# Performance work log

Hardware: AMD Instinct MI355X
Metric: run time of the kernel (lower is better)

## Reference

```python
import jax, jax.numpy as jnp
import numpy as np

# ---- p4m group tables (g = 4*m + r, m in {0,1} mirror, r in {0..3} rot90) ----
def _p4m_tables():
    R = np.array([[0, -1], [1, 0]])
    F = np.array([[-1, 0], [0, 1]])
    I = np.eye(2, dtype=int)
    mats = []
    for m in (0, 1):
        for r in range(4):
            mats.append(np.linalg.matrix_power(R, r) @ (F if m else I))
    def idx(M):
        for i, A in enumerate(mats):
            if np.array_equal(A, M):
                return i
        raise ValueError('not in group')
    comp = np.array([[idx(mats[a] @ mats[b]) for b in range(8)] for a in range(8)])
    inv = np.array([idx(mats[a].T) for a in range(8)])  # orthogonal -> inv = transpose
    return comp, inv

COMP, INV = _p4m_tables()

def _transform_kernel(g, W):
    # L_g applied to filter spatial axes: mirror (last axis) then rotate r times
    m, r = g // 4, g % 4
    if m:
        W = jnp.flip(W, axis=-1)
    return jnp.rot90(W, k=r, axes=(-2, -1))

STRIDE, PADDING, DILATION = 1, 1, 1

def setup_inputs() -> dict:
    key = jax.random.key(0)
    k1, k2 = jax.random.split(key)
    B, Cin, Cout, H, W, kH, kW = 16, 64, 64, 64, 64, 3, 3
    x = jax.random.normal(k1, (B, Cin, 8, H, W), dtype=jnp.float32)
    scale = 1.0 / np.sqrt(Cin * kH * kW)
    weight_rel = jax.random.normal(k2, (Cout, Cin, 8, kH, kW), dtype=jnp.float32) * scale
    bias = jnp.zeros((Cout,), dtype=jnp.float32)
    return {'x': x, 'weight_rel': weight_rel, 'bias': bias}

def _gconv(x, weight_rel, bias):
    B, Cin, N, H, Wd = x.shape  # N == 8
    Cout, _, _, kH, kW = weight_rel.shape
    # Build the full group-equivariant filter bank once (fused form of the
    # original 64 small conv2d calls): bank[g*Cout+co, c*8+h] = L_g psi(g^{-1} h)
    banks = []
    for g in range(8):
        u = COMP[INV[g]]                # [8] relative element u = g^{-1} h, for h=0..7
        Wg = weight_rel[:, :, u]        # [Cout, Cin, 8, kH, kW]
        banks.append(_transform_kernel(g, Wg))
    bank = jnp.stack(banks, 0)          # [8, Cout, Cin, 8, kH, kW]
    bank = bank.reshape(8 * Cout, Cin * 8, kH, kW)
    x2 = x.reshape(B, Cin * 8, H, Wd)   # in-channel index = c*8 + h, matches bank
    y = jax.lax.conv_general_dilated(
        x2, bank,
        window_strides=(STRIDE, STRIDE),
        padding=[(PADDING, PADDING), (PADDING, PADDING)],
        rhs_dilation=(DILATION, DILATION),
        dimension_numbers=('NCHW', 'OIHW', 'NCHW'))
    Ho, Wo = y.shape[-2], y.shape[-1]
    y = y.reshape(B, 8, Cout, Ho, Wo).transpose(0, 2, 1, 3, 4)  # [B, Cout, 8, Ho, Wo]
    return y + bias[None, :, None, None, None]

def reference(x, weight_rel, bias):
    return _gconv(x, weight_rel, bias)
```

## Files before the change

### kernel.cpp

```cpp
#include <hip/hip_runtime.h>
#include <stdint.h>

typedef short  bf16x8 __attribute__((ext_vector_type(8)));
typedef float  f32x4  __attribute__((ext_vector_type(4)));


__device__ __forceinline__ short f2bf(float f) {
    uint32_t u = __builtin_bit_cast(uint32_t, f);
    u += 0x7FFFu + ((u >> 16) & 1u);
    return (short)(u >> 16);
}

__device__ __forceinline__ int u_index(int g, int s) {
    int r  = g & 3, m  = g >> 2;
    int r2 = s & 3, ms = s >> 2;
    if (!m) { int rr = (r2 - r) & 3; return ms ? (4 + rr) : rr; }
    else    { int rr = (r - r2) & 3; return ms ? rr : (4 + rr); }
}

__device__ __forceinline__ void gload_lds16(const void* g, void* l) {
    __builtin_amdgcn_global_load_lds(
        (const __attribute__((address_space(1))) uint32_t*)g,
        (__attribute__((address_space(3))) uint32_t*)l, 16, 0, 0);
}

#define XB_BYTES  (16LL * 66 * 66 * 512 * 2)
#define BK_BYTES  (16LL * 9 * 4 * 512 * 8 * 2)
#define WS_NEEDED (XB_BYTES + BK_BYTES)


__global__ __launch_bounds__(256) void prep_x2(const float* __restrict__ x,
                                               short* __restrict__ xb) {
    __shared__ float t[64][65];
    const int h = blockIdx.x, kc8 = blockIdx.y, b = blockIdx.z;
    const int k0 = kc8 * 64;
    const int tid = threadIdx.x;
    const int w  = tid & 63, kq = tid >> 6;
    const float* xp = x + ((size_t)(b * 512 + k0 + kq) * 4096) + h * 64 + w;
    #pragma unroll
    for (int i = 0; i < 16; ++i)
        t[kq + 4 * i][w] = xp[(size_t)(4 * i) * 4096];
    __syncthreads();
    const int w2 = tid >> 3, kk = tid & 7;
    #pragma unroll
    for (int half = 0; half < 2; ++half) {
        const int ww = w2 + 32 * half;
        bf16x8 v;
        #pragma unroll
        for (int j = 0; j < 8; ++j) v[j] = f2bf(t[kk * 8 + j][ww]);
        size_t o = (((size_t)b * 66 + h + 1) * 66 + (ww + 1)) * 512 + k0 + kk * 8;
        *reinterpret_cast<bf16x8*>(&xb[o]) = v;
    }
}

__global__ __launch_bounds__(256) void zero_border(short* __restrict__ xb) {
    int idx = blockIdx.x * 256 + threadIdx.x;
    if (idx >= 16 * 260 * 64) return;
    int kg = idx & 63;
    int rest = idx >> 6;
    int b  = rest / 260;
    int pe = rest - b * 260;
    int hh, ww;
    if      (pe < 66)  { hh = 0;            ww = pe; }
    else if (pe < 132) { hh = 65;           ww = pe - 66; }
    else if (pe < 196) { hh = pe - 132 + 1; ww = 0; }
    else               { hh = pe - 196 + 1; ww = 65; }
    size_t o = (((size_t)b * 66 + hh) * 66 + ww) * 512 + kg * 8;
    bf16x8 z = {0,0,0,0,0,0,0,0};
    *reinterpret_cast<bf16x8*>(&xb[o]) = z;
}

__global__ __launch_bounds__(256) void prep_w(const float* __restrict__ wrel,
                                              short* __restrict__ bank) {
    int tg = blockIdx.x * 256 + threadIdx.x;
    int oc = tg & 511;
    int kg = (tg >> 9) & 3;
    int kc = (tg >> 11) & 15;
    int t  = tg >> 15;
    int ki = t / 3, kj = t - ki * 3;
    int g = oc & 7, co = oc >> 3;
    int r = g & 3, m = g >> 2;
    int a0, b0;
    switch (r) {
        case 0:  a0 = ki;     b0 = kj;     break;
        case 1:  a0 = kj;     b0 = 2 - ki; break;
        case 2:  a0 = 2 - ki; b0 = 2 - kj; break;
        default: a0 = 2 - kj; b0 = ki;     break;
    }
    if (m) b0 = 2 - b0;
    int ci = kc * 4 + kg;
    const float* wp = wrel + (size_t)(co * 64 + ci) * 72 + a0 * 3 + b0;
    bf16x8 v;
    #pragma unroll
    for (int j = 0; j < 8; ++j) v[j] = f2bf(wp[u_index(g, j) * 9]);
    size_t o = (((((size_t)kc * 3 + kj) * 3 + ki) * 4 + kg) * 512 + oc) * 8;
    *reinterpret_cast<bf16x8*>(&bank[o]) = v;
}

#define XS_SH (1344 * 8)
#define WB_SH (768 * 8)

#define STAGE_X(XS, kc)                                                    \
    {                                                                      \
        _Pragma("unroll")                                                  \
        for (int q = 0; q < 6; ++q) {                                      \
            int it = wid + 4 * q;                                          \
            if (it < 21)                                                   \
                gload_lds16(xb + (size_t)xoff[q] + (kc) * 32,              \
                            &XS[it * 512]);                                \
        }                                                                  \
    }

#define STAGE_W(WB, kc, kj)                                                \
    {                                                                      \
        _Pragma("unroll")                                                  \
        for (int q = 0; q < 3; ++q) {                                      \
            int it = wid + 4 * q;                                          \
            gload_lds16(bank + (size_t)((kc) * 3 + (kj)) * 49152           \
                             + woff[q],                                    \
                        &WB[it * 512]);                                    \
        }                                                                  \
    }

#define COMPUTE_KJ(XS, WB, kj)                                             \
    {                                                                      \
        bf16x8 bfr[6];                                                     \
        _Pragma("unroll")                                                  \
        for (int rr = 0; rr < 6; ++rr)                                     \
            bfr[rr] = *reinterpret_cast<const bf16x8*>(                    \
                &XS[(lkg * 336 + (wid * 4 + rr) * 18 + l15 + (kj)) * 8]);  \
        _Pragma("unroll")                                                  \
        for (int ki = 0; ki < 3; ++ki) {                                   \
            bf16x8 a[4];                                                   \
            _Pragma("unroll")                                              \
            for (int mi = 0; mi < 4; ++mi)                                 \
                a[mi] = *reinterpret_cast<const bf16x8*>(                  \
                    &WB[((ki * 4 + lkg) * 64 + mi * 16 + l15) * 8]);       \
            _Pragma("unroll")                                              \
            for (int nj = 0; nj < 4; ++nj) {                               \
                bf16x8 bv = bfr[nj + ki];                                  \
                _Pragma("unroll")                                          \
                for (int mi = 0; mi < 4; ++mi)                             \
                    acc[mi][nj] = __builtin_amdgcn_mfma_f32_16x16x32_bf16( \
                        a[mi], bv, acc[mi][nj], 0, 0, 0);                  \
            }                                                              \
        }                                                                  \
    }

#define CHUNK(kc, XC, XN, W0, W1)                                          \
    {                                                                      \
        STAGE_W(W1, kc, 1);                                                \
        COMPUTE_KJ(XC, W0, 0);                                             \
        __syncthreads();                                                   \
        STAGE_W(W0, kc, 2);                                                \
        if ((kc) < 15) STAGE_X(XN, (kc) + 1);                              \
        COMPUTE_KJ(XC, W1, 1);                                             \
        __syncthreads();                                                   \
        if ((kc) < 15) STAGE_W(W1, (kc) + 1, 0);                           \
        COMPUTE_KJ(XC, W0, 2);                                             \
        __syncthreads();                                                   \
    }

__global__ __launch_bounds__(256, 2) void gconv_mfma(
    const short* __restrict__ xb, const short* __restrict__ bank,
    const float* __restrict__ bias, float* __restrict__ out)
{
    __shared__ __attribute__((aligned(16))) short xsA[XS_SH], xsB[XS_SH];
    __shared__ __attribute__((aligned(16))) short wbA[WB_SH], wbB[WB_SH];

    const int st  = blockIdx.x;
    const int ot  = blockIdx.y;
    const int b   = blockIdx.z;
    const int h0  = (st >> 2) * 16;
    const int w0  = (st & 3) * 16;
    const int oc0 = ot * 64;

    const int tid  = threadIdx.x;
    const int lane = tid & 63;
    const int wid  = tid >> 6;
    const int l15  = lane & 15;
    const int lkg  = lane >> 4;

    f32x4 acc[4][4];
    #pragma unroll
    for (int i = 0; i < 4; ++i)
        #pragma unroll
        for (int j = 0; j < 4; ++j)
            #pragma unroll
            for (int e = 0; e < 4; ++e) acc[i][j][e] = 0.f;

    const int xrow_base = (b * 66 + h0) * 66 + w0;

    int xoff[6];
    #pragma unroll
    for (int q = 0; q < 6; ++q) {
        int it = wid + 4 * q;
        if (it > 20) it = 20;
        int slot = it * 64 + lane;
        int kg = slot / 336;
        int px = slot - kg * 336;
        px = px < 324 ? px : 323;
        int r = px / 18;
        int c = px - r * 18;
        xoff[q] = (xrow_base + r * 66 + c) * 512 + kg * 8;
    }
    int woff[3];
    #pragma unroll
    for (int q = 0; q < 3; ++q) {
        int it = wid + 4 * q;
        woff[q] = (it * 512 + oc0 + lane) * 8;
    }

    STAGE_X(xsA, 0);
    STAGE_W(wbA, 0, 0);
    __syncthreads();
    for (int kc2 = 0; kc2 < 8; ++kc2) {
        CHUNK(2 * kc2,     xsA, xsB, wbA, wbB);
        CHUNK(2 * kc2 + 1, xsB, xsA, wbB, wbA);
    }

    #pragma unroll
    for (int mi = 0; mi < 4; ++mi) {
        #pragma unroll
        for (int j = 0; j < 4; ++j) {
            const int oc_g = oc0 + mi * 16 + lkg * 4 + j;
            const float bv = bias[oc_g >> 3];
            float* op = out + ((size_t)b * 512 + oc_g) * 4096;
            #pragma unroll
            for (int nj = 0; nj < 4; ++nj) {
                const int hh = h0 + wid * 4 + nj;
                op[hh * 64 + w0 + l15] = acc[mi][nj][j] + bv;
            }
        }
    }
}

__global__ __launch_bounds__(256) void gconv_direct(
    const float* __restrict__ x, const float* __restrict__ wrel,
    const float* __restrict__ bias, float* __restrict__ out)
{
    __shared__ float xsf[18][20];
    __shared__ float wsf[16][9];
    const int st = blockIdx.x, ct = blockIdx.y, b = blockIdx.z;
    const int h0 = (st >> 2) * 16, w0 = (st & 3) * 16, oc0 = ct * 16;
    const int tid = threadIdx.x;
    const int ch = tid & 15, blk = tid >> 4;
    const int by = (blk >> 2) * 4, bx = (blk & 3) * 4;
    const int oc = oc0 + ch, g = oc & 7, co = oc >> 3;
    const int wl_c = tid / 9, wl_k = tid - wl_c * 9;
    const int wl_i = wl_k / 3, wl_j = wl_k - wl_i * 3;
    const int wl_oc = oc0 + wl_c, wl_g = wl_oc & 7, wl_co = wl_oc >> 3;
    int a0, b0;
    { const int r = wl_g & 3, m = wl_g >> 2;
      switch (r) { case 0: a0=wl_i; b0=wl_j; break; case 1: a0=wl_j; b0=2-wl_i; break;
                   case 2: a0=2-wl_i; b0=2-wl_j; break; default: a0=2-wl_j; b0=wl_i; break; }
      if (m) b0 = 2 - b0; }
    float acc[4][4];
    #pragma unroll
    for (int i=0;i<4;++i) for (int j=0;j<4;++j) acc[i][j]=0.f;
    for (int t = 0; t < 512; ++t) {
        const int ci = t >> 3, s = t & 7;
        __syncthreads();
        const float* xp = x + (((size_t)(b * 64 + ci) * 8 + s) * 4096);
        for (int idx = tid; idx < 18 * 18; idx += 256) {
            const int rr = idx / 18, cc = idx - rr * 18;
            const int gh = h0 - 1 + rr, gw = w0 - 1 + cc;
            float v = 0.f;
            if (gh >= 0 && gh < 64 && gw >= 0 && gw < 64) v = xp[gh * 64 + gw];
            xsf[rr][cc] = v;
        }
        if (tid < 144) {
            const int u = u_index(wl_g, s);
            wsf[wl_c][wl_k] = wrel[((size_t)(wl_co*64+ci)*8+u)*9 + a0*3 + b0];
        }
        __syncthreads();
        float wr[9];
        #pragma unroll
        for (int k=0;k<9;++k) wr[k]=wsf[ch][k];
        float xv[6][6];
        #pragma unroll
        for (int i=0;i<6;++i) for (int j=0;j<6;++j) xv[i][j]=xsf[by+i][bx+j];
        #pragma unroll
        for (int py=0;py<4;++py) for (int px=0;px<4;++px)
            for (int ki=0;ki<3;++ki) for (int kj=0;kj<3;++kj)
                acc[py][px] += xv[py+ki][px+kj]*wr[ki*3+kj];
    }
    const float bv = bias[co];
    float* op = out + (((size_t)(b*64+co)*8+g)*4096);
    #pragma unroll
    for (int py=0;py<4;++py) for (int px=0;px<4;++px)
        op[(h0+by+py)*64 + (w0+bx+px)] = acc[py][px] + bv;
}

extern "C" void kernel_launch(void* const* d_in, const int* in_sizes, int n_in,
                              void* d_out, int out_size, void* d_ws, size_t ws_size,
                              hipStream_t stream) {
    const float* x    = (const float*)d_in[0];
    const float* wrel = (const float*)d_in[1];
    const float* bias = (const float*)d_in[2];
    float* out        = (float*)d_out;

    if (ws_size >= (size_t)WS_NEEDED) {
        short* xb   = (short*)d_ws;
        short* bank = (short*)((char*)d_ws + XB_BYTES);
        zero_border<<<1040, 256, 0, stream>>>(xb);
        {
            dim3 g(64, 8, 16);
            prep_x2<<<g, 256, 0, stream>>>(x, xb);
        }
        prep_w<<<1152, 256, 0, stream>>>(wrel, bank);
        dim3 grid(16, 8, 16);
        gconv_mfma<<<grid, 256, 0, stream>>>(xb, bank, bias, out);
    } else {
        dim3 grid(16, 32, 16);
        gconv_direct<<<grid, 256, 0, stream>>>(x, wrel, bias, out);
    }
}
```

Measured before the change: 301.7 us.

## Triple-buffer weight tiles with counted vmcnt waits and MFMA priority boosts

Replaces the double-buffered weight LDS tiles with three per-kj buffers and reorders staging so the next chunk's X tile and weights are issued one or two phases ahead. Full __syncthreads are replaced by explicit s_waitcnt vmcnt(N) plus s_barrier, so only the needed loads are waited on. s_setprio raises wave priority around the MFMA loops. Out-of-range X loads are now clamped instead of branched, which issues redundant duplicate loads in exchange for uniform vmcnt accounting. LDS use grows, which may affect the 2-blocks-per-CU occupancy.

New measurement: 317.3 us. 5.2% more time.

```diff
diff --git a/kernel.cpp b/kernel.cpp
--- a/kernel.cpp
+++ b/kernel.cpp
@@ -97,17 +97,17 @@
     *reinterpret_cast<bf16x8*>(&bank[o]) = v;
 }
 
-#define XS_SH (1344 * 8)
-#define WB_SH (768 * 8)
+#define XS_SH (21 * 512)
+#define WJ_SH (12 * 512)
 
 #define STAGE_X(XS, kc)                                                    \
     {                                                                      \
         _Pragma("unroll")                                                  \
         for (int q = 0; q < 6; ++q) {                                      \
             int it = wid + 4 * q;                                          \
-            if (it < 21)                                                   \
-                gload_lds16(xb + (size_t)xoff[q] + (kc) * 32,              \
-                            &XS[it * 512]);                                \
+            int dst = it > 20 ? 20 : it;                                   \
+            gload_lds16(xb + (size_t)xoff[q] + (kc) * 32,                  \
+                        &XS[dst * 512]);                                   \
         }                                                                  \
     }
 
@@ -129,6 +129,7 @@
         for (int rr = 0; rr < 6; ++rr)                                     \
             bfr[rr] = *reinterpret_cast<const bf16x8*>(                    \
                 &XS[(lkg * 336 + (wid * 4 + rr) * 18 + l15 + (kj)) * 8]);  \
+        __builtin_amdgcn_s_setprio(1);                                     \
         _Pragma("unroll")                                                  \
         for (int ki = 0; ki < 3; ++ki) {                                   \
             bf16x8 a[4];                                                   \
@@ -145,20 +146,27 @@
                         a[mi], bv, acc[mi][nj], 0, 0, 0);                  \
             }                                                              \
         }                                                                  \
-    }
-
-#define CHUNK(kc, XC, XN, W0, W1)                                          \
+        __builtin_amdgcn_s_setprio(0);                                     \
+    }
+
+#define PHASE_END(N)                                                       \
+    asm volatile("s_waitcnt vmcnt(" #N ")" ::: "memory");                  \
+    __builtin_amdgcn_s_barrier();                                          \
+    __builtin_amdgcn_sched_barrier(0);
+
+#define CHUNK(kc, XC, XN)                                                  \
     {                                                                      \
-        STAGE_W(W1, kc, 1);                                                \
-        COMPUTE_KJ(XC, W0, 0);                                             \
-        __syncthreads();                                                   \
-        STAGE_W(W0, kc, 2);                                                \
-        if ((kc) < 15) STAGE_X(XN, (kc) + 1);                              \
-        COMPUTE_KJ(XC, W1, 1);                                             \
-        __syncthreads();                                                   \
-        if ((kc) < 15) STAGE_W(W1, (kc) + 1, 0);                           \
-        COMPUTE_KJ(XC, W0, 2);                                             \
-        __syncthreads();                                                   \
+        const int kcn = ((kc) < 15) ? (kc) + 1 : 15;                       \
+        STAGE_X(XN, kcn);                                                  \
+        STAGE_W(wj2, kc, 2);                                               \
+        COMPUTE_KJ(XC, wj0, 0);                                            \
+        PHASE_END(9)                                                       \
+        STAGE_W(wj0, kcn, 0);                                              \
+        COMPUTE_KJ(XC, wj1, 1);                                            \
+        PHASE_END(3)                                                       \
+        STAGE_W(wj1, kcn, 1);                                              \
+        COMPUTE_KJ(XC, wj2, 2);                                            \
+        PHASE_END(3)                                                       \
     }
 
 __global__ __launch_bounds__(256, 2) void gconv_mfma(
@@ -166,7 +174,8 @@
     const float* __restrict__ bias, float* __restrict__ out)
 {
     __shared__ __attribute__((aligned(16))) short xsA[XS_SH], xsB[XS_SH];
-    __shared__ __attribute__((aligned(16))) short wbA[WB_SH], wbB[WB_SH];
+    __shared__ __attribute__((aligned(16))) short wj0[WJ_SH], wj1[WJ_SH],
+                                                  wj2[WJ_SH];
 
     const int st  = blockIdx.x;
     const int ot  = blockIdx.y;
@@ -212,11 +221,13 @@
     }
 
     STAGE_X(xsA, 0);
-    STAGE_W(wbA, 0, 0);
-    __syncthreads();
+    STAGE_W(wj0, 0, 0);
+    STAGE_W(wj1, 0, 1);
+    PHASE_END(3)
+
     for (int kc2 = 0; kc2 < 8; ++kc2) {
-        CHUNK(2 * kc2,     xsA, xsB, wbA, wbB);
-        CHUNK(2 * kc2 + 1, xsB, xsA, wbB, wbA);
+        CHUNK(2 * kc2,     xsA, xsB);
+        CHUNK(2 * kc2 + 1, xsB, xsA);
     }
 
     #pragma unroll
```

## Load weight fragments directly from global memory instead of staging through LDS

Applied to the files above, without the earlier changes.

Removes the LDS double-buffered weight tiles and reads the MFMA A-operand fragments straight from global/L2 per (kc, tap). The bank layout is reindexed by tap t so the per-lane address is a simple stride. This frees LDS, cuts synchronisations from three to one per chunk, and raises launch bounds to three blocks per CU. The cost is per-wave global weight loads in the inner loop whose latency may not be hidden, plus redundant weight traffic across waves.

Result: slower. 347.8 us (+15.3%).

```diff
diff --git a/kernel.cpp b/kernel.cpp
--- a/kernel.cpp
+++ b/kernel.cpp
@@ -93,12 +93,11 @@
     bf16x8 v;
     #pragma unroll
     for (int j = 0; j < 8; ++j) v[j] = f2bf(wp[u_index(g, j) * 9]);
-    size_t o = (((((size_t)kc * 3 + kj) * 3 + ki) * 4 + kg) * 512 + oc) * 8;
+    size_t o = ((((size_t)kc * 9 + t) * 4 + kg) * 512 + oc) * 8;
     *reinterpret_cast<bf16x8*>(&bank[o]) = v;
 }
 
-#define XS_SH (1344 * 8)
-#define WB_SH (768 * 8)
+#define XS_SH (21 * 512)
 
 #define STAGE_X(XS, kc)                                                    \
     {                                                                      \
@@ -111,62 +110,40 @@
         }                                                                  \
     }
 
-#define STAGE_W(WB, kc, kj)                                                \
+#define COMPUTE_CHUNK(XS, kc)                                              \
     {                                                                      \
         _Pragma("unroll")                                                  \
-        for (int q = 0; q < 3; ++q) {                                      \
-            int it = wid + 4 * q;                                          \
-            gload_lds16(bank + (size_t)((kc) * 3 + (kj)) * 49152           \
-                             + woff[q],                                    \
-                        &WB[it * 512]);                                    \
-        }                                                                  \
-    }
-
-#define COMPUTE_KJ(XS, WB, kj)                                             \
-    {                                                                      \
-        bf16x8 bfr[6];                                                     \
-        _Pragma("unroll")                                                  \
-        for (int rr = 0; rr < 6; ++rr)                                     \
-            bfr[rr] = *reinterpret_cast<const bf16x8*>(                    \
-                &XS[(lkg * 336 + (wid * 4 + rr) * 18 + l15 + (kj)) * 8]);  \
-        _Pragma("unroll")                                                  \
-        for (int ki = 0; ki < 3; ++ki) {                                   \
-            bf16x8 a[4];                                                   \
+        for (int kj = 0; kj < 3; ++kj) {                                   \
+            bf16x8 bfr[6];                                                 \
             _Pragma("unroll")                                              \
-            for (int mi = 0; mi < 4; ++mi)                                 \
-                a[mi] = *reinterpret_cast<const bf16x8*>(                  \
-                    &WB[((ki * 4 + lkg) * 64 + mi * 16 + l15) * 8]);       \
+            for (int rr = 0; rr < 6; ++rr)                                 \
+                bfr[rr] = *reinterpret_cast<const bf16x8*>(                \
+                    &XS[(lkg * 336 + (wid * 4 + rr) * 18 + l15 + (kj)) * 8]); \
             _Pragma("unroll")                                              \
-            for (int nj = 0; nj < 4; ++nj) {                               \
-                bf16x8 bv = bfr[nj + ki];                                  \
+            for (int ki = 0; ki < 3; ++ki) {                               \
+                const int t = ki * 3 + kj;                                 \
+                bf16x8 a[4];                                               \
                 _Pragma("unroll")                                          \
                 for (int mi = 0; mi < 4; ++mi)                             \
-                    acc[mi][nj] = __builtin_amdgcn_mfma_f32_16x16x32_bf16( \
-                        a[mi], bv, acc[mi][nj], 0, 0, 0);                  \
+                    a[mi] = *reinterpret_cast<const bf16x8*>(              \
+                        wbase + (size_t)((kc) * 9 + t) * 16384 + mi * 128); \
+                _Pragma("unroll")                                          \
+                for (int nj = 0; nj < 4; ++nj) {                           \
+                    bf16x8 bv = bfr[nj + ki];                              \
+                    _Pragma("unroll")                                      \
+                    for (int mi = 0; mi < 4; ++mi)                         \
+                        acc[mi][nj] = __builtin_amdgcn_mfma_f32_16x16x32_bf16( \
+                            a[mi], bv, acc[mi][nj], 0, 0, 0);              \
+                }                                                          \
             }                                                              \
         }                                                                  \
     }
 
-#define CHUNK(kc, XC, XN, W0, W1)                                          \
-    {                                                                      \
-        STAGE_W(W1, kc, 1);                                                \
-        COMPUTE_KJ(XC, W0, 0);                                             \
-        __syncthreads();                                                   \
-        STAGE_W(W0, kc, 2);                                                \
-        if ((kc) < 15) STAGE_X(XN, (kc) + 1);                              \
-        COMPUTE_KJ(XC, W1, 1);                                             \
-        __syncthreads();                                                   \
-        if ((kc) < 15) STAGE_W(W1, (kc) + 1, 0);                           \
-        COMPUTE_KJ(XC, W0, 2);                                             \
-        __syncthreads();                                                   \
-    }
-
-__global__ __launch_bounds__(256, 2) void gconv_mfma(
+__global__ __launch_bounds__(256, 3) void gconv_mfma(
     const short* __restrict__ xb, const short* __restrict__ bank,
     const float* __restrict__ bias, float* __restrict__ out)
 {
     __shared__ __attribute__((aligned(16))) short xsA[XS_SH], xsB[XS_SH];
-    __shared__ __attribute__((aligned(16))) short wbA[WB_SH], wbB[WB_SH];
 
     const int st  = blockIdx.x;
     const int ot  = blockIdx.y;
@@ -180,6 +157,8 @@
     const int wid  = tid >> 6;
     const int l15  = lane & 15;
     const int lkg  = lane >> 4;
+
+    const short* wbase = bank + lkg * 4096 + (size_t)(oc0 + l15) * 8;
 
     f32x4 acc[4][4];
     #pragma unroll
@@ -204,19 +183,16 @@
         int c = px - r * 18;
         xoff[q] = (xrow_base + r * 66 + c) * 512 + kg * 8;
     }
-    int woff[3];
-    #pragma unroll
-    for (int q = 0; q < 3; ++q) {
-        int it = wid + 4 * q;
-        woff[q] = (it * 512 + oc0 + lane) * 8;
-    }
 
     STAGE_X(xsA, 0);
-    STAGE_W(wbA, 0, 0);
     __syncthreads();
     for (int kc2 = 0; kc2 < 8; ++kc2) {
-        CHUNK(2 * kc2,     xsA, xsB, wbA, wbB);
-        CHUNK(2 * kc2 + 1, xsB, xsA, wbB, wbA);
+        STAGE_X(xsB, 2 * kc2 + 1);
+        COMPUTE_CHUNK(xsA, 2 * kc2);
+        __syncthreads();
+        if (kc2 < 7) STAGE_X(xsA, 2 * kc2 + 2);
+        COMPUTE_CHUNK(xsB, 2 * kc2 + 1);
+        __syncthreads();
     }
 
     #pragma unroll
```

## Triple-buffer weight tiles and register-double-buffer MFMA fragments across LDS reads

Applied to the files above, without the earlier changes.

Replaces the two alternating weight LDS buffers with three buffers, one per kernel column kj. It also splits compute into a fragment prefetch from LDS into registers and an MFMA burst. Two fragment sets alternate, so the LDS reads for the next kj step are issued while the current step's MFMAs run, and the global-to-LDS staging is reordered to match. This is meant to hide LDS read latency behind matrix work, at the cost of more registers and LDS per block, which could limit occupancy. The last chunk now issues redundant staging loads instead of branching.

Measured after the change: 294.2 us. 1.03x faster.

```diff
diff --git a/kernel.cpp b/kernel.cpp
--- a/kernel.cpp
+++ b/kernel.cpp
@@ -97,8 +97,10 @@
     *reinterpret_cast<bf16x8*>(&bank[o]) = v;
 }
 
-#define XS_SH (1344 * 8)
-#define WB_SH (768 * 8)
+#define XS_SH (21 * 512)
+#define WB_SH (12 * 512)
+
+struct FragSet { bf16x8 b[6]; bf16x8 a[3][4]; };
 
 #define STAGE_X(XS, kc)                                                    \
     {                                                                      \
@@ -122,42 +124,49 @@
         }                                                                  \
     }
 
-#define COMPUTE_KJ(XS, WB, kj)                                             \
-    {                                                                      \
-        bf16x8 bfr[6];                                                     \
+#define PREFETCH(R, XS, WB, kj)                                            \
+    {                                                                      \
         _Pragma("unroll")                                                  \
         for (int rr = 0; rr < 6; ++rr)                                     \
-            bfr[rr] = *reinterpret_cast<const bf16x8*>(                    \
+            R.b[rr] = *reinterpret_cast<const bf16x8*>(                    \
                 &XS[(lkg * 336 + (wid * 4 + rr) * 18 + l15 + (kj)) * 8]);  \
         _Pragma("unroll")                                                  \
-        for (int ki = 0; ki < 3; ++ki) {                                   \
-            bf16x8 a[4];                                                   \
+        for (int ki = 0; ki < 3; ++ki)                                     \
             _Pragma("unroll")                                              \
             for (int mi = 0; mi < 4; ++mi)                                 \
-                a[mi] = *reinterpret_cast<const bf16x8*>(                  \
+                R.a[ki][mi] = *reinterpret_cast<const bf16x8*>(            \
                     &WB[((ki * 4 + lkg) * 64 + mi * 16 + l15) * 8]);       \
+    }
+
+#define MFMA_BURST(R)                                                      \
+    {                                                                      \
+        _Pragma("unroll")                                                  \
+        for (int ki = 0; ki < 3; ++ki)                                     \
             _Pragma("unroll")                                              \
             for (int nj = 0; nj < 4; ++nj) {                               \
-                bf16x8 bv = bfr[nj + ki];                                  \
+                bf16x8 bv = R.b[nj + ki];                                  \
                 _Pragma("unroll")                                          \
                 for (int mi = 0; mi < 4; ++mi)                             \
                     acc[mi][nj] = __builtin_amdgcn_mfma_f32_16x16x32_bf16( \
-                        a[mi], bv, acc[mi][nj], 0, 0, 0);                  \
+                        R.a[ki][mi], bv, acc[mi][nj], 0, 0, 0);            \
             }                                                              \
-        }                                                                  \
-    }
-
-#define CHUNK(kc, XC, XN, W0, W1)                                          \
-    {                                                                      \
-        STAGE_W(W1, kc, 1);                                                \
-        COMPUTE_KJ(XC, W0, 0);                                             \
+    }
+
+#define CHUNK(kc, XC, XN, RA, RB)                                          \
+    {                                                                      \
+        const int kcn = ((kc) < 15) ? (kc) + 1 : 15;                       \
+        STAGE_W(wb2, kc, 2);                                               \
+        STAGE_X(XN, kcn);                                                  \
+        PREFETCH(RB, XC, wb1, 1);                                          \
+        MFMA_BURST(RA);                                                    \
         __syncthreads();                                                   \
-        STAGE_W(W0, kc, 2);                                                \
-        if ((kc) < 15) STAGE_X(XN, (kc) + 1);                              \
-        COMPUTE_KJ(XC, W1, 1);                                             \
+        STAGE_W(wb0, kcn, 0);                                              \
+        PREFETCH(RA, XC, wb2, 2);                                          \
+        MFMA_BURST(RB);                                                    \
         __syncthreads();                                                   \
-        if ((kc) < 15) STAGE_W(W1, (kc) + 1, 0);                           \
-        COMPUTE_KJ(XC, W0, 2);                                             \
+        STAGE_W(wb1, kcn, 1);                                              \
+        PREFETCH(RB, XN, wb0, 0);                                          \
+        MFMA_BURST(RA);                                                    \
         __syncthreads();                                                   \
     }
 
@@ -166,7 +175,8 @@
     const float* __restrict__ bias, float* __restrict__ out)
 {
     __shared__ __attribute__((aligned(16))) short xsA[XS_SH], xsB[XS_SH];
-    __shared__ __attribute__((aligned(16))) short wbA[WB_SH], wbB[WB_SH];
+    __shared__ __attribute__((aligned(16))) short wb0[WB_SH], wb1[WB_SH],
+                                                  wb2[WB_SH];
 
     const int st  = blockIdx.x;
     const int ot  = blockIdx.y;
@@ -211,12 +221,17 @@
         woff[q] = (it * 512 + oc0 + lane) * 8;
     }
 
+    FragSet fsA, fsB;
+
     STAGE_X(xsA, 0);
-    STAGE_W(wbA, 0, 0);
+    STAGE_W(wb0, 0, 0);
+    STAGE_W(wb1, 0, 1);
     __syncthreads();
+    PREFETCH(fsA, xsA, wb0, 0);
+
     for (int kc2 = 0; kc2 < 8; ++kc2) {
-        CHUNK(2 * kc2,     xsA, xsB, wbA, wbB);
-        CHUNK(2 * kc2 + 1, xsB, xsA, wbB, wbA);
+        CHUNK(2 * kc2,     xsA, xsB, fsA, fsB);
+        CHUNK(2 * kc2 + 1, xsB, xsA, fsB, fsA);
     }
 
     #pragma unroll
```
